# Performance work log

Measured on AMD Instinct MI355X. Metric: run time of the kernel, lower is better.

## Reference

```python
import jax, jax.numpy as jnp
import numpy as np


def setup_inputs() -> dict:
    key = jax.random.key(0)
    ks = jax.random.split(key, 6)
    B, H, W, C = 4, 64, 64, 256
    D = 256  # d_model
    s = 0.02
    return {
        "features": jax.random.normal(ks[0], (B, H, W, C), dtype=jnp.float32),
        "Wq": jax.random.normal(ks[1], (C, D), dtype=jnp.float32) * s,
        "bq": jnp.zeros((D,), dtype=jnp.float32),
        "Wk": jax.random.normal(ks[2], (C, D), dtype=jnp.float32) * s,
        "bk": jnp.zeros((D,), dtype=jnp.float32),
        "Wv": jax.random.normal(ks[3], (C, D), dtype=jnp.float32) * s,
        "bv": jnp.zeros((D,), dtype=jnp.float32),
        "Wo": jax.random.normal(ks[4], (D, C), dtype=jnp.float32) * s,
        "bo": jnp.zeros((C,), dtype=jnp.float32),
    }


def reference(features, Wq, bq, Wk, bk, Wv, bv, Wo, bo):
    # features: [B, H, W, C] (NHWC). 1x1 convs are per-pixel GEMMs, so flatten
    # spatial dims to N = H*W tokens and do single-head self-attention.
    B, H, W, C = features.shape
    D = Wq.shape[1]
    x = features.reshape(B, H * W, C)          # [B, N, C]
    q = x @ Wq + bq                            # [B, N, D]
    k = x @ Wk + bk                            # [B, N, D]
    v = x @ Wv + bv                            # [B, N, D]
    scale = np.float32(1.0 / np.sqrt(D))
    scores = jnp.einsum("bnd,bmd->bnm", q, k) * scale   # [B, N, N]
    attn = jax.nn.softmax(scores, axis=-1)               # [B, N, N]
    out = jnp.einsum("bnm,bmd->bnd", attn, v)            # [B, N, D]
    out = out @ Wo + bo                                  # [B, N, C]
    return out.reshape(B, H, W, C)
```

## Files before the change

### kernel.cpp

```cpp
#include <hip/hip_runtime.h>
#include <hip/hip_bf16.h>


typedef __attribute__((ext_vector_type(8))) short short8;
typedef __attribute__((ext_vector_type(4))) short short4v;
typedef __attribute__((ext_vector_type(4))) float floatx4;

#define NB 4
#define NT 4096
#define CD 256
#define MTOT (NB * NT)

__device__ __forceinline__ short bf16s(float f) {
    union { float f; unsigned u; } a; a.f = f;
    unsigned u = a.u;
    return (short)((u + 0x7fffu + ((u >> 16) & 1u)) >> 16);
}

__device__ __forceinline__ float bf2f(short s) {
    union { unsigned u; float f; } a;
    a.u = ((unsigned)(unsigned short)s) << 16;
    return a.f;
}

__device__ __forceinline__ short8 ld8(const short* p) {
    return *(const short8*)p;
}

__device__ __forceinline__ floatx4 mfma16(short8 a, short8 b, floatx4 c) {
    return __builtin_amdgcn_mfma_f32_16x16x32_bf16(a, b, c, 0, 0, 0);
}

__device__ __forceinline__ void dma16(const void* g, void* l) {
    __builtin_amdgcn_global_load_lds(
        (const __attribute__((address_space(1))) void*)g,
        (__attribute__((address_space(3))) void*)l, 16, 0, 0);
}

__global__ __launch_bounds__(256) void k_convx(const float* __restrict__ x,
                                               short* __restrict__ xb) {
    int i = (blockIdx.x * 256 + threadIdx.x) * 4;
    float4 v = *(const float4*)(x + i);
    short4v o;
    o.x = bf16s(v.x); o.y = bf16s(v.y); o.z = bf16s(v.z); o.w = bf16s(v.w);
    *(short4v*)(xb + i) = o;
}

__global__ __launch_bounds__(256) void k_convw(const float* __restrict__ w0,
                                               const float* __restrict__ w1,
                                               const float* __restrict__ w2,
                                               const float* __restrict__ w3,
                                               short* __restrict__ wt) {
    int z = blockIdx.y;
    const float* w = (z == 0) ? w0 : (z == 1) ? w1 : (z == 2) ? w2 : w3;
    int c = blockIdx.x;
    int n = threadIdx.x;
    wt[z * 65536 + n * 256 + c] = bf16s(w[c * 256 + n]);
}

__global__ __launch_bounds__(256) void k_proj3(const short* __restrict__ A,
                                               const short* __restrict__ Wt,
                                               const float* __restrict__ bq,
                                               const float* __restrict__ bk,
                                               const float* __restrict__ bv,
                                               short* __restrict__ Qb,
                                               short* __restrict__ Kb,
                                               short* __restrict__ Vt) {
    __shared__ __align__(16) short Ws[16384];
    int z = blockIdx.z;
    const short* W = Wt + z * 65536;
    const float* bias = (z == 0) ? bq : (z == 1) ? bk : bv;
    float scale = (z == 0) ? 0.0625f : 1.0f;
    int m0 = blockIdx.x * 128;
    int n0 = blockIdx.y * 64;
    int tid = threadIdx.x;
    int w = tid >> 6, l = tid & 63, r = l & 15, q = l >> 4;

#pragma unroll
    for (int cg = 0; cg < 8; ++cg)
        dma16(W + (size_t)(n0 + w * 16 + r) * CD + (cg * 4 + q) * 8,
              &Ws[w * 4096 + cg * 512]);
    __syncthreads();

    const short* a0 = A + (size_t)(m0 + w * 32 + r) * CD;
    const short* a1 = a0 + 16 * CD;
    floatx4 acc[2][4];
#pragma unroll
    for (int rt = 0; rt < 2; ++rt)
#pragma unroll
        for (int j = 0; j < 4; ++j) acc[rt][j] = (floatx4){0.f, 0.f, 0.f, 0.f};
#pragma unroll
    for (int c = 0; c < 8; ++c) {
        short8 af0 = ld8(a0 + c * 32 + q * 8);
        short8 af1 = ld8(a1 + c * 32 + q * 8);
#pragma unroll
        for (int j = 0; j < 4; ++j) {
            short8 wf = ld8(&Ws[j * 4096 + c * 512 + l * 8]);
            acc[0][j] = mfma16(af0, wf, acc[0][j]);
            acc[1][j] = mfma16(af1, wf, acc[1][j]);
        }
    }
#pragma unroll
    for (int rt = 0; rt < 2; ++rt)
#pragma unroll
        for (int j = 0; j < 4; ++j) {
            int col = n0 + j * 16 + r;
            float bvv = bias[col];
#pragma unroll
            for (int i = 0; i < 4; ++i) {
                int row = m0 + w * 32 + rt * 16 + q * 4 + i;
                short s = bf16s((acc[rt][j][i] + bvv) * scale);
                if (z == 0) Qb[(size_t)row * CD + col] = s;
                else if (z == 1) Kb[(size_t)row * CD + col] = s;
                else {
                    int bb = row >> 12, lm = row & (NT - 1);
                    Vt[((size_t)bb * CD + col) * NT + lm] = s;
                }
            }
        }
}

__global__ __launch_bounds__(512, 4) void k_attn(const short* __restrict__ Qb,
                                                 const short* __restrict__ Kb,
                                                 const short* __restrict__ Vt,
                                                 short* __restrict__ Op0,
                                                 short* __restrict__ Op1,
                                                 float* __restrict__ Lp) {
    __shared__ __align__(16) short Ks[2][16384];
    __shared__ __align__(16) short P[64][68];

    const int tid = threadIdx.x;
    const int w = tid >> 6;
    const int l = tid & 63;
    const int r = l & 15, q = l >> 4;
    const int rg = w & 3;
    const int th = w >> 2;
    const int b = blockIdx.y;
    const int ks = blockIdx.z;
    const int m0 = blockIdx.x * 64;
    const int t0 = ks * 2048;
    const int tt_d = w & 3;
    const int cb_d = (w >> 2) * 4;
    const short* Qp = Qb + (size_t)b * NT * CD;
    const short* Kp = Kb + (size_t)b * NT * CD;
    const short* Vp = Vt + (size_t)b * CD * NT;
    short* Op = (ks == 0) ? Op0 : Op1;

    short8 qf[8];
#pragma unroll
    for (int c = 0; c < 8; ++c)
        qf[c] = ld8(Qp + (size_t)(m0 + rg * 16 + r) * CD + c * 32 + q * 8);

    floatx4 o[4][2];
#pragma unroll
    for (int rt = 0; rt < 4; ++rt)
#pragma unroll
        for (int dt = 0; dt < 2; ++dt) o[rt][dt] = (floatx4){0.f, 0.f, 0.f, 0.f};
    float ls = 0.f;

#pragma unroll
    for (int j = 0; j < 4; ++j)
        dma16(Kp + (size_t)(t0 + tt_d * 16 + r) * CD + ((cb_d + j) * 4 + q) * 8,
              &Ks[0][tt_d * 4096 + (cb_d + j) * 512]);

#pragma unroll 1
    for (int it = 0; it < 32; ++it) {
        const int p = it & 1;
        const int n0 = t0 + it * 64;
        __syncthreads();

        short8 vf[2][2];
#pragma unroll
        for (int t2 = 0; t2 < 2; ++t2)
#pragma unroll
            for (int dt = 0; dt < 2; ++dt)
                vf[t2][dt] = ld8(Vp + (size_t)(w * 32 + dt * 16 + r) * NT +
                                 n0 + t2 * 32 + q * 8);

        if (it + 1 < 32) {
#pragma unroll
            for (int j = 0; j < 4; ++j)
                dma16(Kp + (size_t)(n0 + 64 + tt_d * 16 + r) * CD + ((cb_d + j) * 4 + q) * 8,
                      &Ks[1 - p][tt_d * 4096 + (cb_d + j) * 512]);
        }

        floatx4 s0 = {0.f, 0.f, 0.f, 0.f};
        floatx4 s1 = {0.f, 0.f, 0.f, 0.f};
#pragma unroll
        for (int c = 0; c < 8; ++c) {
            s0 = mfma16(ld8(&Ks[p][(th * 2 + 0) * 4096 + c * 512 + l * 8]), qf[c], s0);
            s1 = mfma16(ld8(&Ks[p][(th * 2 + 1) * 4096 + c * 512 + l * 8]), qf[c], s1);
        }

#pragma unroll
        for (int tt = 0; tt < 2; ++tt) {
            floatx4 sv = tt ? s1 : s0;
            float e0 = __expf(sv[0]), e1 = __expf(sv[1]);
            float e2 = __expf(sv[2]), e3 = __expf(sv[3]);
            ls += (e0 + e1) + (e2 + e3);
            unsigned pk01, pk23;
            asm("v_cvt_pk_bf16_f32 %0, %1, %2" : "=v"(pk01) : "v"(e0), "v"(e1));
            asm("v_cvt_pk_bf16_f32 %0, %1, %2" : "=v"(pk23) : "v"(e2), "v"(e3));
            uint2 pk; pk.x = pk01; pk.y = pk23;
            *(uint2*)&P[rg * 16 + r][th * 32 + tt * 16 + q * 4] = pk;
        }
        asm volatile("s_waitcnt lgkmcnt(0)\n\ts_barrier" ::: "memory");

#pragma unroll
        for (int rt = 0; rt < 4; ++rt) {
#pragma unroll
            for (int t2 = 0; t2 < 2; ++t2) {
                short8 pf = ld8(&P[rt * 16 + r][t2 * 32 + q * 8]);
                o[rt][0] = mfma16(pf, vf[t2][0], o[rt][0]);
                o[rt][1] = mfma16(pf, vf[t2][1], o[rt][1]);
            }
        }
    }

    ls += __shfl_xor(ls, 16);
    ls += __shfl_xor(ls, 32);
    if (l < 16)
        Lp[(size_t)(ks * 2 + th) * MTOT + b * NT + m0 + rg * 16 + l] = ls;

#pragma unroll
    for (int rt = 0; rt < 4; ++rt)
#pragma unroll
        for (int i = 0; i < 4; ++i) {
            int row = m0 + rt * 16 + q * 4 + i;
#pragma unroll
            for (int dt = 0; dt < 2; ++dt)
                Op[((size_t)b * NT + row) * CD + w * 32 + dt * 16 + r] =
                    bf16s(o[rt][dt][i]);
        }
}

__global__ __launch_bounds__(256) void k_oproj(const short* __restrict__ Op0,
                                               const short* __restrict__ Op1,
                                               const float* __restrict__ Lp,
                                               const short* __restrict__ Wot,
                                               const float* __restrict__ bo,
                                               float* __restrict__ out) {
    __shared__ __align__(16) short Ws[16384];
    int m0 = blockIdx.x * 128;
    int n0 = blockIdx.y * 64;
    int tid = threadIdx.x;
    int w = tid >> 6, l = tid & 63, r = l & 15, q = l >> 4;

#pragma unroll
    for (int cg = 0; cg < 8; ++cg)
        dma16(Wot + (size_t)(n0 + w * 16 + r) * CD + (cg * 4 + q) * 8,
              &Ws[w * 4096 + cg * 512]);
    __syncthreads();

    int row0 = m0 + w * 32 + r;
    float lt0 = (Lp[row0] + Lp[MTOT + row0]) +
                (Lp[2 * MTOT + row0] + Lp[3 * MTOT + row0]);
    float lt1 = (Lp[row0 + 16] + Lp[MTOT + row0 + 16]) +
                (Lp[2 * MTOT + row0 + 16] + Lp[3 * MTOT + row0 + 16]);
    float inv0 = 1.0f / lt0, inv1 = 1.0f / lt1;
    const short* p00 = Op0 + (size_t)row0 * CD;
    const short* p01 = Op1 + (size_t)row0 * CD;
    floatx4 acc[2][4];
#pragma unroll
    for (int rt = 0; rt < 2; ++rt)
#pragma unroll
        for (int j = 0; j < 4; ++j) acc[rt][j] = (floatx4){0.f, 0.f, 0.f, 0.f};
#pragma unroll
    for (int c = 0; c < 8; ++c) {
        int off0 = c * 32 + q * 8, off1 = 16 * CD + c * 32 + q * 8;
        short8 x0 = ld8(p00 + off0), y0 = ld8(p01 + off0);
        short8 x1 = ld8(p00 + off1), y1 = ld8(p01 + off1);
        short8 af0, af1;
#pragma unroll
        for (int jj = 0; jj < 8; ++jj) {
            af0[jj] = bf16s((bf2f(x0[jj]) + bf2f(y0[jj])) * inv0);
            af1[jj] = bf16s((bf2f(x1[jj]) + bf2f(y1[jj])) * inv1);
        }
#pragma unroll
        for (int j = 0; j < 4; ++j) {
            short8 wf = ld8(&Ws[j * 4096 + c * 512 + l * 8]);
            acc[0][j] = mfma16(af0, wf, acc[0][j]);
            acc[1][j] = mfma16(af1, wf, acc[1][j]);
        }
    }
#pragma unroll
    for (int rt = 0; rt < 2; ++rt)
#pragma unroll
        for (int j = 0; j < 4; ++j) {
            int col = n0 + j * 16 + r;
            float bvv = bo[col];
#pragma unroll
            for (int i = 0; i < 4; ++i)
                out[(size_t)(m0 + w * 32 + rt * 16 + q * 4 + i) * CD + col] =
                    acc[rt][j][i] + bvv;
        }
}

extern "C" void kernel_launch(void* const* d_in, const int* in_sizes, int n_in,
                              void* d_out, int out_size, void* d_ws, size_t ws_size,
                              hipStream_t stream) {
    const float* x  = (const float*)d_in[0];
    const float* Wq = (const float*)d_in[1];
    const float* bq = (const float*)d_in[2];
    const float* Wk = (const float*)d_in[3];
    const float* bk = (const float*)d_in[4];
    const float* Wv = (const float*)d_in[5];
    const float* bv = (const float*)d_in[6];
    const float* Wo = (const float*)d_in[7];
    const float* bo = (const float*)d_in[8];
    float* out = (float*)d_out;

    char* ws = (char*)d_ws;
    const size_t MB = 1024u * 1024u;
    short* xb  = (short*)(ws);
    short* Op0 = (short*)(ws);
    short* Qb  = (short*)(ws + 8 * MB);
    short* Kb  = (short*)(ws + 16 * MB);
    short* Vt  = (short*)(ws + 24 * MB);
    short* Op1 = (short*)(ws + 32 * MB);
    short* Wt  = (short*)(ws + 40 * MB);
    float* Lp  = (float*)(ws + 40 * MB + 512 * 1024);

    k_convx<<<dim3(MTOT * CD / (256 * 4)), 256, 0, stream>>>(x, xb);
    k_convw<<<dim3(256, 4), 256, 0, stream>>>(Wq, Wk, Wv, Wo, Wt);
    k_proj3<<<dim3(MTOT / 128, CD / 64, 3), 256, 0, stream>>>(xb, Wt, bq, bk, bv, Qb, Kb, Vt);
    k_attn<<<dim3(NT / 64, NB, 2), 512, 0, stream>>>(Qb, Kb, Vt, Op0, Op1, Lp);
    k_oproj<<<dim3(MTOT / 128, CD / 64), 256, 0, stream>>>(Op0, Op1, Lp, Wt + 196608, bo, out);
}
```

Before: 287.7 us.

## Shrink attention tile to 32 queries and 32 keys per iteration with 4 waves

Retiles the attention kernel from 64 query rows and 512 threads to 32 query rows and 256 threads. Each iteration now processes 32 keys, and each wave owns 64 output dimensions instead of 32. The grid doubles, LDS per block halves and more blocks fit per CU, which is meant to improve occupancy and latency hiding. The cost is that each K/V tile is reused by half as many queries, so global K/V traffic and barriers per unit of work roughly double.

```diff
diff --git a/kernel.cpp b/kernel.cpp
--- a/kernel.cpp
+++ b/kernel.cpp
@@ -120,27 +120,27 @@
         }
 }
 
-__global__ __launch_bounds__(512, 4) void k_attn(const short* __restrict__ Qb,
+__global__ __launch_bounds__(256, 4) void k_attn(const short* __restrict__ Qb,
                                                  const short* __restrict__ Kb,
                                                  const short* __restrict__ Vt,
                                                  short* __restrict__ Op0,
                                                  short* __restrict__ Op1,
                                                  float* __restrict__ Lp) {
-    __shared__ __align__(16) short Ks[2][16384];
-    __shared__ __align__(16) short P[64][68];
+    __shared__ __align__(16) short Ks[2][8192];
+    __shared__ __align__(16) short P[32][36];
 
     const int tid = threadIdx.x;
     const int w = tid >> 6;
     const int l = tid & 63;
     const int r = l & 15, q = l >> 4;
-    const int rg = w & 3;
-    const int th = w >> 2;
+    const int rg = w & 1;
+    const int th = w >> 1;
     const int b = blockIdx.y;
     const int ks = blockIdx.z;
-    const int m0 = blockIdx.x * 64;
+    const int m0 = blockIdx.x * 32;
     const int t0 = ks * 2048;
-    const int tt_d = w & 3;
-    const int cb_d = (w >> 2) * 4;
+    const int tt_d = w & 1;
+    const int cb_d = (w >> 1) * 4;
     const short* Qp = Qb + (size_t)b * NT * CD;
     const short* Kp = Kb + (size_t)b * NT * CD;
     const short* Vp = Vt + (size_t)b * CD * NT;
@@ -151,11 +151,11 @@
     for (int c = 0; c < 8; ++c)
         qf[c] = ld8(Qp + (size_t)(m0 + rg * 16 + r) * CD + c * 32 + q * 8);
 
-    floatx4 o[4][2];
-#pragma unroll
-    for (int rt = 0; rt < 4; ++rt)
-#pragma unroll
-        for (int dt = 0; dt < 2; ++dt) o[rt][dt] = (floatx4){0.f, 0.f, 0.f, 0.f};
+    floatx4 o[2][4];
+#pragma unroll
+    for (int rt = 0; rt < 2; ++rt)
+#pragma unroll
+        for (int dt = 0; dt < 4; ++dt) o[rt][dt] = (floatx4){0.f, 0.f, 0.f, 0.f};
     float ls = 0.f;
 
 #pragma unroll
@@ -164,56 +164,45 @@
               &Ks[0][tt_d * 4096 + (cb_d + j) * 512]);
 
 #pragma unroll 1
-    for (int it = 0; it < 32; ++it) {
+    for (int it = 0; it < 64; ++it) {
         const int p = it & 1;
-        const int n0 = t0 + it * 64;
+        const int n0 = t0 + it * 32;
         __syncthreads();
 
-        short8 vf[2][2];
-#pragma unroll
-        for (int t2 = 0; t2 < 2; ++t2)
-#pragma unroll
-            for (int dt = 0; dt < 2; ++dt)
-                vf[t2][dt] = ld8(Vp + (size_t)(w * 32 + dt * 16 + r) * NT +
-                                 n0 + t2 * 32 + q * 8);
-
-        if (it + 1 < 32) {
+        short8 vf[4];
+#pragma unroll
+        for (int dt = 0; dt < 4; ++dt)
+            vf[dt] = ld8(Vp + (size_t)(w * 64 + dt * 16 + r) * NT + n0 + q * 8);
+
+        if (it + 1 < 64) {
 #pragma unroll
             for (int j = 0; j < 4; ++j)
-                dma16(Kp + (size_t)(n0 + 64 + tt_d * 16 + r) * CD + ((cb_d + j) * 4 + q) * 8,
+                dma16(Kp + (size_t)(n0 + 32 + tt_d * 16 + r) * CD + ((cb_d + j) * 4 + q) * 8,
                       &Ks[1 - p][tt_d * 4096 + (cb_d + j) * 512]);
         }
 
-        floatx4 s0 = {0.f, 0.f, 0.f, 0.f};
-        floatx4 s1 = {0.f, 0.f, 0.f, 0.f};
-#pragma unroll
-        for (int c = 0; c < 8; ++c) {
-            s0 = mfma16(ld8(&Ks[p][(th * 2 + 0) * 4096 + c * 512 + l * 8]), qf[c], s0);
-            s1 = mfma16(ld8(&Ks[p][(th * 2 + 1) * 4096 + c * 512 + l * 8]), qf[c], s1);
-        }
-
-#pragma unroll
-        for (int tt = 0; tt < 2; ++tt) {
-            floatx4 sv = tt ? s1 : s0;
-            float e0 = __expf(sv[0]), e1 = __expf(sv[1]);
-            float e2 = __expf(sv[2]), e3 = __expf(sv[3]);
-            ls += (e0 + e1) + (e2 + e3);
-            unsigned pk01, pk23;
-            asm("v_cvt_pk_bf16_f32 %0, %1, %2" : "=v"(pk01) : "v"(e0), "v"(e1));
-            asm("v_cvt_pk_bf16_f32 %0, %1, %2" : "=v"(pk23) : "v"(e2), "v"(e3));
-            uint2 pk; pk.x = pk01; pk.y = pk23;
-            *(uint2*)&P[rg * 16 + r][th * 32 + tt * 16 + q * 4] = pk;
-        }
+        floatx4 s = {0.f, 0.f, 0.f, 0.f};
+#pragma unroll
+        for (int c = 0; c < 8; ++c)
+            s = mfma16(ld8(&Ks[p][th * 4096 + c * 512 + l * 8]), qf[c], s);
+
+        float e0 = __expf(s[0]), e1 = __expf(s[1]);
+        float e2 = __expf(s[2]), e3 = __expf(s[3]);
+        ls += (e0 + e1) + (e2 + e3);
+        unsigned pk01, pk23;
+        asm("v_cvt_pk_bf16_f32 %0, %1, %2" : "=v"(pk01) : "v"(e0), "v"(e1));
+        asm("v_cvt_pk_bf16_f32 %0, %1, %2" : "=v"(pk23) : "v"(e2), "v"(e3));
+        uint2 pk; pk.x = pk01; pk.y = pk23;
+        *(uint2*)&P[rg * 16 + r][th * 16 + q * 4] = pk;
+
         asm volatile("s_waitcnt lgkmcnt(0)\n\ts_barrier" ::: "memory");
 
 #pragma unroll
-        for (int rt = 0; rt < 4; ++rt) {
-#pragma unroll
-            for (int t2 = 0; t2 < 2; ++t2) {
-                short8 pf = ld8(&P[rt * 16 + r][t2 * 32 + q * 8]);
-                o[rt][0] = mfma16(pf, vf[t2][0], o[rt][0]);
-                o[rt][1] = mfma16(pf, vf[t2][1], o[rt][1]);
-            }
+        for (int rt = 0; rt < 2; ++rt) {
+            short8 pf = ld8(&P[rt * 16 + r][q * 8]);
+#pragma unroll
+            for (int dt = 0; dt < 4; ++dt)
+                o[rt][dt] = mfma16(pf, vf[dt], o[rt][dt]);
         }
     }
 
@@ -223,13 +212,13 @@
         Lp[(size_t)(ks * 2 + th) * MTOT + b * NT + m0 + rg * 16 + l] = ls;
 
 #pragma unroll
-    for (int rt = 0; rt < 4; ++rt)
+    for (int rt = 0; rt < 2; ++rt)
 #pragma unroll
         for (int i = 0; i < 4; ++i) {
             int row = m0 + rt * 16 + q * 4 + i;
 #pragma unroll
-            for (int dt = 0; dt < 2; ++dt)
-                Op[((size_t)b * NT + row) * CD + w * 32 + dt * 16 + r] =
+            for (int dt = 0; dt < 4; ++dt)
+                Op[((size_t)b * NT + row) * CD + w * 64 + dt * 16 + r] =
                     bf16s(o[rt][dt][i]);
         }
 }
@@ -324,6 +313,6 @@
     k_convx<<<dim3(MTOT * CD / (256 * 4)), 256, 0, stream>>>(x, xb);
     k_convw<<<dim3(256, 4), 256, 0, stream>>>(Wq, Wk, Wv, Wo, Wt);
     k_proj3<<<dim3(MTOT / 128, CD / 64, 3), 256, 0, stream>>>(xb, Wt, bq, bk, bv, Qb, Kb, Vt);
-    k_attn<<<dim3(NT / 64, NB, 2), 512, 0, stream>>>(Qb, Kb, Vt, Op0, Op1, Lp);
+    k_attn<<<dim3(NT / 32, NB, 2), 256, 0, stream>>>(Qb, Kb, Vt, Op0, Op1, Lp);
     k_oproj<<<dim3(MTOT / 128, CD / 64), 256, 0, stream>>>(Op0, Op1, Lp, Wt + 196608, bo, out);
 }
```

After: 369.4 us. 28.4% more time.
